# Optimization experiments

Hardware: AMD Instinct MI355X
Metric: run time of the kernel (lower is better)

## Reference

```python
import jax, jax.numpy as jnp
import numpy as np

NUM_NODES = 200000
NUM_GRAPHS = 1024
D_FEAT = 512


def setup_inputs() -> dict:
    key = jax.random.key(0)
    k_x, k_j = jax.random.split(key)
    inputs = jax.random.normal(k_x, (NUM_NODES, D_FEAT), dtype=jnp.float32)
    # Contiguous, strictly-increasing segment start offsets with idx[0] == 0.
    # Base offsets split nodes ~evenly; jitter in [0, step) keeps strict monotonicity.
    step = NUM_NODES // NUM_GRAPHS  # 195
    base = (jnp.arange(NUM_GRAPHS, dtype=jnp.int32) * NUM_NODES) // NUM_GRAPHS
    jitter = jax.random.randint(k_j, (NUM_GRAPHS,), 0, step, dtype=jnp.int32)
    idx = base + jitter
    idx = idx.at[0].set(0)
    return {"inputs": inputs, "idx": idx, "num_nodes": NUM_NODES, "num_graphs": NUM_GRAPHS}


def reference(inputs, idx, num_nodes, num_graphs):
    # Original: dense [num_graphs, num_nodes] pooling matrix with row i holding
    # 1/(idx[i+1]-idx[i]) over columns idx[i]:idx[i+1], then matmul + relu.
    # Equivalent math: per-contiguous-segment mean of node features, then relu.
    node_ids = jnp.arange(num_nodes, dtype=jnp.int32)
    # segment id of node n: largest i with idx[i] <= n (idx[0]=0 -> seg >= 0)
    seg = jnp.searchsorted(idx, node_ids, side="right") - 1  # [num_nodes]
    sums = jax.ops.segment_sum(inputs, seg, num_segments=num_graphs)  # [G, D]
    idx_aug = jnp.append(idx, jnp.int32(num_nodes))
    counts = (idx_aug[1:] - idx_aug[:-1]).astype(inputs.dtype)  # [G]
    out = sums / counts[:, None]
    return jax.nn.relu(out)
```

## Files before the change

kernel.cpp:

```cpp
#include <hip/hip_runtime.h>


#define D_FEAT 512
#define NCOL4 (D_FEAT / 4)

__global__ __launch_bounds__(512) void seg_mean_relu_kernel(
    const float4* __restrict__ in,
    const int* __restrict__ idx,
    float4* __restrict__ out,
    int num_nodes, int num_graphs) {
  const int b = blockIdx.x;
  if (b >= num_graphs) return;

  const int start = idx[b];
  const int end = (b + 1 < num_graphs) ? idx[b + 1] : num_nodes;

  const int col = threadIdx.x & (NCOL4 - 1);
  const int grp = threadIdx.x >> 7;

  float4 acc = make_float4(0.f, 0.f, 0.f, 0.f);
  for (int r = start + grp; r < end; r += 4) {
    float4 v = in[(size_t)r * NCOL4 + col];
    acc.x += v.x;
    acc.y += v.y;
    acc.z += v.z;
    acc.w += v.w;
  }

  __shared__ float4 part[3][NCOL4];
  if (grp > 0) part[grp - 1][col] = acc;
  __syncthreads();

  if (grp == 0) {
#pragma unroll
    for (int g = 0; g < 3; ++g) {
      float4 p = part[g][col];
      acc.x += p.x;
      acc.y += p.y;
      acc.z += p.z;
      acc.w += p.w;
    }
    const int cnt = end - start;
    const float s = (cnt > 0) ? (1.0f / (float)cnt) : 0.0f;
    float4 o;
    o.x = fmaxf(acc.x * s, 0.0f);
    o.y = fmaxf(acc.y * s, 0.0f);
    o.z = fmaxf(acc.z * s, 0.0f);
    o.w = fmaxf(acc.w * s, 0.0f);
    out[(size_t)b * NCOL4 + col] = o;
  }
}

extern "C" void kernel_launch(void* const* d_in, const int* in_sizes, int n_in,
                              void* d_out, int out_size, void* d_ws, size_t ws_size,
                              hipStream_t stream) {
  const float4* in = (const float4*)d_in[0];
  const int* idx = (const int*)d_in[1];
  float4* out = (float4*)d_out;

  const int num_nodes = in_sizes[0] / D_FEAT;
  const int num_graphs = in_sizes[1];

  seg_mean_relu_kernel<<<dim3(num_graphs), dim3(512), 0, stream>>>(
      in, idx, out, num_nodes, num_graphs);
}
```

Before: 89.95 us.

## Balance segment-mean work with equal row chunks and atomic accumulation

Replaces one-block-per-segment scheduling with fixed row ranges per block. Each block binary-searches its starting segment and accumulates partial sums into the output with float atomics. A zero-init kernel runs first and a finalize kernel applies the mean scaling and ReLU afterward. The aim is to remove load imbalance from uneven segment sizes, at the cost of two extra launches, atomic traffic and non-deterministic summation order.

```diff
diff --git a/kernel.cpp b/kernel.cpp
--- a/kernel.cpp
+++ b/kernel.cpp
@@ -4,63 +4,110 @@
 #define D_FEAT 512
 #define NCOL4 (D_FEAT / 4)
 
-__global__ __launch_bounds__(512) void seg_mean_relu_kernel(
+__global__ __launch_bounds__(256) void zero_out_kernel(float4* __restrict__ out,
+                                                       int n4) {
+  int i = blockIdx.x * blockDim.x + threadIdx.x;
+  if (i < n4) out[i] = make_float4(0.f, 0.f, 0.f, 0.f);
+}
+
+__global__ __launch_bounds__(512) void seg_accum_kernel(
     const float4* __restrict__ in,
     const int* __restrict__ idx,
-    float4* __restrict__ out,
-    int num_nodes, int num_graphs) {
-  const int b = blockIdx.x;
-  if (b >= num_graphs) return;
-
-  const int start = idx[b];
-  const int end = (b + 1 < num_graphs) ? idx[b + 1] : num_nodes;
+    float* __restrict__ out,
+    int num_nodes, int num_graphs, int rows_per_blk) {
+  const int r0 = blockIdx.x * rows_per_blk;
+  if (r0 >= num_nodes) return;
+  const int r1 = min(r0 + rows_per_blk, num_nodes);
 
   const int col = threadIdx.x & (NCOL4 - 1);
   const int grp = threadIdx.x >> 7;
 
-  float4 acc = make_float4(0.f, 0.f, 0.f, 0.f);
-  for (int r = start + grp; r < end; r += 4) {
-    float4 v = in[(size_t)r * NCOL4 + col];
-    acc.x += v.x;
-    acc.y += v.y;
-    acc.z += v.z;
-    acc.w += v.w;
+  int lo = 0, hi = num_graphs - 1;
+  while (lo < hi) {
+    int mid = (lo + hi + 1) >> 1;
+    if (idx[mid] <= r0) lo = mid;
+    else hi = mid - 1;
   }
+  int s = lo;
+  int row = r0;
 
   __shared__ float4 part[3][NCOL4];
-  if (grp > 0) part[grp - 1][col] = acc;
-  __syncthreads();
 
-  if (grp == 0) {
+  while (row < r1) {
+    const int seg_end = (s + 1 < num_graphs) ? idx[s + 1] : num_nodes;
+    const int e = min(seg_end, r1);
+
+    float4 acc = make_float4(0.f, 0.f, 0.f, 0.f);
+    for (int r = row + grp; r < e; r += 4) {
+      float4 v = in[(size_t)r * NCOL4 + col];
+      acc.x += v.x;
+      acc.y += v.y;
+      acc.z += v.z;
+      acc.w += v.w;
+    }
+
+    if (grp > 0) part[grp - 1][col] = acc;
+    __syncthreads();
+    if (grp == 0) {
 #pragma unroll
-    for (int g = 0; g < 3; ++g) {
-      float4 p = part[g][col];
-      acc.x += p.x;
-      acc.y += p.y;
-      acc.z += p.z;
-      acc.w += p.w;
+      for (int g = 0; g < 3; ++g) {
+        float4 p = part[g][col];
+        acc.x += p.x;
+        acc.y += p.y;
+        acc.z += p.z;
+        acc.w += p.w;
+      }
+      float* o = out + (size_t)s * D_FEAT + col * 4;
+      atomicAdd(o + 0, acc.x);
+      atomicAdd(o + 1, acc.y);
+      atomicAdd(o + 2, acc.z);
+      atomicAdd(o + 3, acc.w);
     }
-    const int cnt = end - start;
-    const float s = (cnt > 0) ? (1.0f / (float)cnt) : 0.0f;
-    float4 o;
-    o.x = fmaxf(acc.x * s, 0.0f);
-    o.y = fmaxf(acc.y * s, 0.0f);
-    o.z = fmaxf(acc.z * s, 0.0f);
-    o.w = fmaxf(acc.w * s, 0.0f);
-    out[(size_t)b * NCOL4 + col] = o;
+    __syncthreads();
+
+    row = e;
+    ++s;
   }
 }
 
+__global__ __launch_bounds__(256) void finalize_kernel(
+    float* __restrict__ out, const int* __restrict__ idx, int num_nodes,
+    int num_graphs) {
+  int i = blockIdx.x * blockDim.x + threadIdx.x;
+  int total4 = num_graphs * NCOL4;
+  if (i >= total4) return;
+  int g = i >> 7;
+  int start = idx[g];
+  int end = (g + 1 < num_graphs) ? idx[g + 1] : num_nodes;
+  float sInv = 1.0f / (float)(end - start);
+  float4* o4 = (float4*)out;
+  float4 v = o4[i];
+  v.x = fmaxf(v.x * sInv, 0.f);
+  v.y = fmaxf(v.y * sInv, 0.f);
+  v.z = fmaxf(v.z * sInv, 0.f);
+  v.w = fmaxf(v.w * sInv, 0.f);
+  o4[i] = v;
+}
+
 extern "C" void kernel_launch(void* const* d_in, const int* in_sizes, int n_in,
-                              void* d_out, int out_size, void* d_ws, size_t ws_size,
-                              hipStream_t stream) {
+                              void* d_out, int out_size, void* d_ws,
+                              size_t ws_size, hipStream_t stream) {
   const float4* in = (const float4*)d_in[0];
   const int* idx = (const int*)d_in[1];
-  float4* out = (float4*)d_out;
+  float* out = (float*)d_out;
 
   const int num_nodes = in_sizes[0] / D_FEAT;
   const int num_graphs = in_sizes[1];
 
-  seg_mean_relu_kernel<<<dim3(num_graphs), dim3(512), 0, stream>>>(
-      in, idx, out, num_nodes, num_graphs);
+  const int out4 = num_graphs * NCOL4;
+  zero_out_kernel<<<dim3((out4 + 255) / 256), dim3(256), 0, stream>>>(
+      (float4*)out, out4);
+
+  const int nblocks = 1024;
+  const int rows_per_blk = (num_nodes + nblocks - 1) / nblocks;
+  seg_accum_kernel<<<dim3(nblocks), dim3(512), 0, stream>>>(
+      in, idx, out, num_nodes, num_graphs, rows_per_blk);
+
+  finalize_kernel<<<dim3((out4 + 255) / 256), dim3(256), 0, stream>>>(
+      out, idx, num_nodes, num_graphs);
 }
```

Result: no change. 88.82 us (-1.3%).
